# Performance work log

Measured on AMD Instinct MI355X. Metric: run time of the kernel, lower is better.

## Reference

```python
import jax, jax.numpy as jnp
import numpy as np

V = 32000   # vocab_size
K = 3       # k-gram context length
D = 1024    # embed_size (also MLP hidden dim)
S = 2048    # seq_len
B = 2       # batch


def setup_inputs() -> dict:
    key = jax.random.key(0)
    k_tok, k_e, k_w1, k_b1, k_w2, k_b2 = jax.random.split(key, 6)
    tokens_seq = jax.random.randint(k_tok, (S, B), 0, V, dtype=jnp.int64)
    scale_emb = 0.02
    embedding = jax.random.normal(k_e, (V, D), dtype=jnp.float32) * scale_emb
    # torch Linear default init: U(-1/sqrt(fan_in), 1/sqrt(fan_in))
    lim1 = 1.0 / np.sqrt(K * D)
    W1 = jax.random.uniform(k_w1, (K * D, D), jnp.float32, -lim1, lim1)
    b1 = jax.random.uniform(k_b1, (D,), jnp.float32, -lim1, lim1)
    lim2 = 1.0 / np.sqrt(D)
    W2 = jax.random.uniform(k_w2, (D, V), jnp.float32, -lim2, lim2)
    b2 = jax.random.uniform(k_b2, (V,), jnp.float32, -lim2, lim2)
    return {"tokens_seq": tokens_seq, "embedding": embedding,
            "W1": W1, "b1": b1, "W2": W2, "b2": b2}


def reference(tokens_seq, embedding, W1, b1, W2, b2):
    # Context for position t = tokens [t-K .. t-1], left-padded with token id 0.
    # Pad K zeros at the front along time: padded[t+j] = tokens[t-K+j].
    padded = jnp.concatenate(
        [jnp.zeros((K, tokens_seq.shape[1]), dtype=tokens_seq.dtype), tokens_seq], axis=0)
    # ctx: (S, B, K) — j-th column is token at offset t-K+j
    ctx = jnp.stack([padded[j:j + S] for j in range(K)], axis=-1)
    # Gather embeddings: (S, B, K, D) -> flatten context to (S, B, K*D)
    emb = embedding[ctx].reshape(S, tokens_seq.shape[1], K * D)
    h = jax.nn.silu(emb @ W1 + b1)          # (S, B, D)
    logits = h @ W2 + b2                     # (S, B, V)
    return logits
```

## Files before the change

### kernel.cpp

```cpp
#include <hip/hip_runtime.h>
#include <hip/hip_bf16.h>

#define V_SZ 32000
#define KCTX 3
#define D_SZ 1024
#define S_SZ 2048
#define B_SZ 2
#define M_SZ (S_SZ * B_SZ)
#define KD   (KCTX * D_SZ)

using bf16x8 = __attribute__((ext_vector_type(8))) __bf16;
using f32x4  = __attribute__((ext_vector_type(4))) float;

__global__ void transpose_cvt(const float* __restrict__ src,
                              __hip_bfloat16* __restrict__ dst,
                              int R, int C) {
    __shared__ float tile[32][33];
    const int c0 = blockIdx.x * 32;
    const int r0 = blockIdx.y * 32;
    const int tx = threadIdx.x;
    const int ty = threadIdx.y;
#pragma unroll
    for (int j = ty; j < 32; j += 8)
        tile[j][tx] = src[(size_t)(r0 + j) * C + (c0 + tx)];
    __syncthreads();
#pragma unroll
    for (int j = ty; j < 32; j += 8)
        dst[(size_t)(c0 + j) * R + (r0 + tx)] = __float2bfloat16(tile[tx][j]);
}

__global__ void gather_cvt(const int* __restrict__ tokens,
                           const float* __restrict__ emb,
                           __hip_bfloat16* __restrict__ X) {
    const int bid = blockIdx.x;
    const int m = bid / KCTX;
    const int j = bid - m * KCTX;
    const int t = m >> 1;
    const int b = m & 1;
    const int tj = t - KCTX + j;
    const int tok = (tj >= 0) ? tokens[tj * B_SZ + b] : 0;

    const float4 v = reinterpret_cast<const float4*>(emb + (size_t)tok * D_SZ)[threadIdx.x];
    __hip_bfloat16 o[4];
    o[0] = __float2bfloat16(v.x);
    o[1] = __float2bfloat16(v.y);
    o[2] = __float2bfloat16(v.z);
    o[3] = __float2bfloat16(v.w);
    __hip_bfloat16* dst = X + (size_t)m * KD + (size_t)j * D_SZ;
    reinterpret_cast<ushort4*>(dst)[threadIdx.x] = *reinterpret_cast<ushort4*>(o);
}

#define TM 128
#define TN 128
#define TK 64

template <int EPI>
__global__ __launch_bounds__(256) void gemm_bt(
    const unsigned short* __restrict__ A,
    const unsigned short* __restrict__ BT,
    const float* __restrict__ bias,
    void* __restrict__ C, int M, int N, int K) {
    __shared__ unsigned short lsA[TM * TK];
    __shared__ unsigned short lsB[TN * TK];

    const int tid  = threadIdx.x;
    const int lane = tid & 63;
    const int w    = tid >> 6;
    const int wm   = (w >> 1) * 64;
    const int wn   = (w & 1) * 64;
    const int m0   = blockIdx.y * TM;
    const int n0   = blockIdx.x * TN;

    f32x4 acc[4][4] = {};

    for (int k0 = 0; k0 < K; k0 += TK) {
        __syncthreads();
#pragma unroll
        for (int i = 0; i < 4; ++i) {
            const int s = i * 256 + tid;
            const int r = s >> 3;
            const int c = s & 7;
            const unsigned short* srcA = A + (size_t)(m0 + r) * K + k0 + c * 8;
            __builtin_amdgcn_global_load_lds(
                (const __attribute__((address_space(1))) void*)srcA,
                (__attribute__((address_space(3))) void*)(lsA + s * 8), 16, 0, 0);
            const unsigned short* srcB = BT + (size_t)(n0 + r) * K + k0 + c * 8;
            __builtin_amdgcn_global_load_lds(
                (const __attribute__((address_space(1))) void*)srcB,
                (__attribute__((address_space(3))) void*)(lsB + s * 8), 16, 0, 0);
        }
        __syncthreads();

#pragma unroll
        for (int kk = 0; kk < 2; ++kk) {
            const int kb = kk * 32 + (lane >> 4) * 8;
            bf16x8 a[4], b[4];
#pragma unroll
            for (int mi = 0; mi < 4; ++mi)
                a[mi] = *reinterpret_cast<const bf16x8*>(
                    &lsA[(wm + mi * 16 + (lane & 15)) * TK + kb]);
#pragma unroll
            for (int ni = 0; ni < 4; ++ni)
                b[ni] = *reinterpret_cast<const bf16x8*>(
                    &lsB[(wn + ni * 16 + (lane & 15)) * TK + kb]);
#pragma unroll
            for (int mi = 0; mi < 4; ++mi)
#pragma unroll
                for (int ni = 0; ni < 4; ++ni)
                    acc[mi][ni] = __builtin_amdgcn_mfma_f32_16x16x32_bf16(
                        a[mi], b[ni], acc[mi][ni], 0, 0, 0);
        }
    }

    const int cn    = n0 + wn + (lane & 15);
    const int rbase = m0 + wm + (lane >> 4) * 4;
#pragma unroll
    for (int mi = 0; mi < 4; ++mi) {
#pragma unroll
        for (int ni = 0; ni < 4; ++ni) {
            const int col = cn + ni * 16;
            const float bv = bias[col];
#pragma unroll
            for (int r = 0; r < 4; ++r) {
                const int row = rbase + mi * 16 + r;
                const float x = acc[mi][ni][r] + bv;
                if (EPI == 0) {
                    const float s = x / (1.0f + __expf(-x));
                    reinterpret_cast<__hip_bfloat16*>(C)[(size_t)row * N + col] =
                        __float2bfloat16(s);
                } else {
                    reinterpret_cast<float*>(C)[(size_t)row * N + col] = x;
                }
            }
        }
    }
}

extern "C" void kernel_launch(void* const* d_in, const int* in_sizes, int n_in,
                              void* d_out, int out_size, void* d_ws, size_t ws_size,
                              hipStream_t stream) {
    const int*   tokens = (const int*)d_in[0];
    const float* emb    = (const float*)d_in[1];
    const float* W1     = (const float*)d_in[2];
    const float* b1     = (const float*)d_in[3];
    const float* W2     = (const float*)d_in[4];
    const float* b2     = (const float*)d_in[5];
    float* out = (float*)d_out;

    char* ws = (char*)d_ws;
    __hip_bfloat16* W2T = (__hip_bfloat16*)(ws);
    __hip_bfloat16* W1T = (__hip_bfloat16*)(ws + 65536000);
    __hip_bfloat16* X   = (__hip_bfloat16*)(ws + 71827456);
    __hip_bfloat16* H   = (__hip_bfloat16*)(ws + 96993280);

    transpose_cvt<<<dim3(V_SZ / 32, D_SZ / 32), dim3(32, 8), 0, stream>>>(W2, W2T, D_SZ, V_SZ);
    transpose_cvt<<<dim3(D_SZ / 32, KD / 32), dim3(32, 8), 0, stream>>>(W1, W1T, KD, D_SZ);
    gather_cvt<<<M_SZ * KCTX, 256, 0, stream>>>(tokens, emb, X);
    gemm_bt<0><<<dim3(D_SZ / TN, M_SZ / TM), 256, 0, stream>>>(
        (const unsigned short*)X, (const unsigned short*)W1T, b1, H, M_SZ, D_SZ, KD);
    gemm_bt<1><<<dim3(V_SZ / TN, M_SZ / TM), 256, 0, stream>>>(
        (const unsigned short*)H, (const unsigned short*)W2T, b2, out, M_SZ, V_SZ, D_SZ);
}
```

Measured before the change: 1.105 ms.

## Factor first GEMM per token and combine shifted partials; remap workgroups for XCD locality

Rather than gathering a 3-token context and running a K=3072 GEMM, each token's embedding is gathered once and multiplied by all three W1 slices (N=3072, K=1024). A combine kernel then sums the shifted per-position partial outputs, adds the bias and applies SiLU. This cuts the gather traffic and makes the first GEMM's inner dimension shorter, at the cost of a large fp32 intermediate Y and an extra pass. The GEMM grid is also flattened and block ids are swizzled so that tiles are grouped per XCD.

```diff
diff --git a/kernel.cpp b/kernel.cpp
--- a/kernel.cpp
+++ b/kernel.cpp
@@ -8,13 +8,17 @@
 #define B_SZ 2
 #define M_SZ (S_SZ * B_SZ)
 #define KD   (KCTX * D_SZ)
+#define M1   (M_SZ + 128)
 
 using bf16x8 = __attribute__((ext_vector_type(8))) __bf16;
 using f32x4  = __attribute__((ext_vector_type(4))) float;
 
-__global__ void transpose_cvt(const float* __restrict__ src,
-                              __hip_bfloat16* __restrict__ dst,
+__global__ void transpose_cvt(const float* __restrict__ src0,
+                              __hip_bfloat16* __restrict__ dst0,
                               int R, int C) {
+    const size_t zoff = (size_t)blockIdx.z * R * C;
+    const float* src = src0 + zoff;
+    __hip_bfloat16* dst = dst0 + zoff;
     __shared__ float tile[32][33];
     const int c0 = blockIdx.x * 32;
     const int r0 = blockIdx.y * 32;
@@ -29,25 +33,44 @@
         dst[(size_t)(c0 + j) * R + (r0 + tx)] = __float2bfloat16(tile[tx][j]);
 }
 
-__global__ void gather_cvt(const int* __restrict__ tokens,
-                           const float* __restrict__ emb,
-                           __hip_bfloat16* __restrict__ X) {
-    const int bid = blockIdx.x;
-    const int m = bid / KCTX;
-    const int j = bid - m * KCTX;
-    const int t = m >> 1;
-    const int b = m & 1;
-    const int tj = t - KCTX + j;
-    const int tok = (tj >= 0) ? tokens[tj * B_SZ + b] : 0;
-
+__global__ void gather1(const int* __restrict__ tokens,
+                        const float* __restrict__ emb,
+                        __hip_bfloat16* __restrict__ A1) {
+    const int m = blockIdx.x;
+    const int tok = (m < M_SZ) ? tokens[m] : 0;
     const float4 v = reinterpret_cast<const float4*>(emb + (size_t)tok * D_SZ)[threadIdx.x];
     __hip_bfloat16 o[4];
     o[0] = __float2bfloat16(v.x);
     o[1] = __float2bfloat16(v.y);
     o[2] = __float2bfloat16(v.z);
     o[3] = __float2bfloat16(v.w);
-    __hip_bfloat16* dst = X + (size_t)m * KD + (size_t)j * D_SZ;
-    reinterpret_cast<ushort4*>(dst)[threadIdx.x] = *reinterpret_cast<ushort4*>(o);
+    reinterpret_cast<ushort4*>(A1 + (size_t)m * D_SZ)[threadIdx.x] =
+        *reinterpret_cast<ushort4*>(o);
+}
+
+__global__ void combine_silu(const float* __restrict__ Y,
+                             const float* __restrict__ b1,
+                             __hip_bfloat16* __restrict__ H) {
+    const int m = blockIdx.x;
+    const int d4 = threadIdx.x;
+    const int r0 = (m >= 6) ? m - 6 : M_SZ;
+    const int r1 = (m >= 4) ? m - 4 : M_SZ;
+    const int r2 = (m >= 2) ? m - 2 : M_SZ;
+    const float4* Yv = reinterpret_cast<const float4*>(Y);
+    const float4 y0 = Yv[(size_t)r0 * 768 + d4];
+    const float4 y1 = Yv[(size_t)r1 * 768 + 256 + d4];
+    const float4 y2 = Yv[(size_t)r2 * 768 + 512 + d4];
+    const float4 bb = reinterpret_cast<const float4*>(b1)[d4];
+    float x[4] = {y0.x + y1.x + y2.x + bb.x, y0.y + y1.y + y2.y + bb.y,
+                  y0.z + y1.z + y2.z + bb.z, y0.w + y1.w + y2.w + bb.w};
+    __hip_bfloat16 o[4];
+#pragma unroll
+    for (int i = 0; i < 4; ++i) {
+        const float s = x[i] / (1.0f + __expf(-x[i]));
+        o[i] = __float2bfloat16(s);
+    }
+    reinterpret_cast<ushort4*>(H + (size_t)m * D_SZ)[d4] =
+        *reinterpret_cast<ushort4*>(o);
 }
 
 #define TM 128
@@ -59,7 +82,7 @@
     const unsigned short* __restrict__ A,
     const unsigned short* __restrict__ BT,
     const float* __restrict__ bias,
-    void* __restrict__ C, int M, int N, int K) {
+    float* __restrict__ C, int M, int N, int K) {
     __shared__ unsigned short lsA[TM * TK];
     __shared__ unsigned short lsB[TN * TK];
 
@@ -68,8 +91,15 @@
     const int w    = tid >> 6;
     const int wm   = (w >> 1) * 64;
     const int wn   = (w & 1) * 64;
-    const int m0   = blockIdx.y * TM;
-    const int n0   = blockIdx.x * TN;
+
+    const int nwg  = gridDim.x;
+    const int q    = nwg >> 3;
+    const int wgid = (blockIdx.x & 7) * q + (blockIdx.x >> 3);
+    const int mt   = M >> 7;
+    const int m_tile = wgid % mt;
+    const int n_tile = wgid / mt;
+    const int m0 = m_tile * TM;
+    const int n0 = n_tile * TN;
 
     f32x4 acc[4][4] = {};
 
@@ -119,18 +149,11 @@
 #pragma unroll
         for (int ni = 0; ni < 4; ++ni) {
             const int col = cn + ni * 16;
-            const float bv = bias[col];
+            const float bv = (EPI == 1) ? bias[col] : 0.0f;
 #pragma unroll
             for (int r = 0; r < 4; ++r) {
                 const int row = rbase + mi * 16 + r;
-                const float x = acc[mi][ni][r] + bv;
-                if (EPI == 0) {
-                    const float s = x / (1.0f + __expf(-x));
-                    reinterpret_cast<__hip_bfloat16*>(C)[(size_t)row * N + col] =
-                        __float2bfloat16(s);
-                } else {
-                    reinterpret_cast<float*>(C)[(size_t)row * N + col] = x;
-                }
+                C[(size_t)row * N + col] = acc[mi][ni][r] + bv;
             }
         }
     }
@@ -148,16 +171,18 @@
     float* out = (float*)d_out;
 
     char* ws = (char*)d_ws;
+    __hip_bfloat16* A1  = (__hip_bfloat16*)(ws);
+    __hip_bfloat16* W1T = (__hip_bfloat16*)(ws + 8650752);
+    float*          Y   = (float*)         (ws + 14942208);
+    __hip_bfloat16* H   = (__hip_bfloat16*)(ws + 66846720);
     __hip_bfloat16* W2T = (__hip_bfloat16*)(ws);
-    __hip_bfloat16* W1T = (__hip_bfloat16*)(ws + 65536000);
-    __hip_bfloat16* X   = (__hip_bfloat16*)(ws + 71827456);
-    __hip_bfloat16* H   = (__hip_bfloat16*)(ws + 96993280);
 
-    transpose_cvt<<<dim3(V_SZ / 32, D_SZ / 32), dim3(32, 8), 0, stream>>>(W2, W2T, D_SZ, V_SZ);
-    transpose_cvt<<<dim3(D_SZ / 32, KD / 32), dim3(32, 8), 0, stream>>>(W1, W1T, KD, D_SZ);
-    gather_cvt<<<M_SZ * KCTX, 256, 0, stream>>>(tokens, emb, X);
-    gemm_bt<0><<<dim3(D_SZ / TN, M_SZ / TM), 256, 0, stream>>>(
-        (const unsigned short*)X, (const unsigned short*)W1T, b1, H, M_SZ, D_SZ, KD);
-    gemm_bt<1><<<dim3(V_SZ / TN, M_SZ / TM), 256, 0, stream>>>(
+    gather1<<<M1, 256, 0, stream>>>(tokens, emb, A1);
+    transpose_cvt<<<dim3(32, 32, 3), dim3(32, 8), 0, stream>>>(W1, W1T, 1024, 1024);
+    gemm_bt<2><<<dim3((KD / TN) * (M1 / TM)), 256, 0, stream>>>(
+        (const unsigned short*)A1, (const unsigned short*)W1T, nullptr, Y, M1, KD, D_SZ);
+    combine_silu<<<M_SZ, 256, 0, stream>>>(Y, b1, H);
+    transpose_cvt<<<dim3(V_SZ / 32, D_SZ / 32, 1), dim3(32, 8), 0, stream>>>(W2, W2T, D_SZ, V_SZ);
+    gemm_bt<1><<<dim3((V_SZ / TN) * (M_SZ / TM)), 256, 0, stream>>>(
         (const unsigned short*)H, (const unsigned short*)W2T, b2, out, M_SZ, V_SZ, D_SZ);
 }
```

New measurement: 1.151 ms. +4.1%, slower.
